# Performance work log

Hardware: AMD Instinct MI355X
Metric: run time of the kernel (lower is better)

The kernel has to match this reference:

```python
import jax, jax.numpy as jnp
import numpy as np

D_MODEL = 1024
N_HEADS = 16
HEAD_DIM = D_MODEL // N_HEADS
WINDOW = 256
NEG_INF = -1e30  # finite stand-in for -inf; identical softmax result, NaN-safe


def setup_inputs() -> dict:
    key = jax.random.key(0)
    ks = jax.random.split(key, 5)
    B, L = 1, 4096
    s = 1.0 / np.sqrt(D_MODEL)
    return {
        "x": jax.random.normal(ks[0], (B, L, D_MODEL), dtype=jnp.float32),
        "Wq": jax.random.normal(ks[1], (D_MODEL, D_MODEL), dtype=jnp.float32) * s,
        "Wk": jax.random.normal(ks[2], (D_MODEL, D_MODEL), dtype=jnp.float32) * s,
        "Wv": jax.random.normal(ks[3], (D_MODEL, D_MODEL), dtype=jnp.float32) * s,
        "Wo": jax.random.normal(ks[4], (D_MODEL, D_MODEL), dtype=jnp.float32) * s,
    }


def reference(x, Wq, Wk, Wv, Wo):
    B, L, _ = x.shape
    # projections (nn.Linear applies x @ W.T; weights here are stored as [out,in])
    q = (x @ Wq.T).reshape(B, L, N_HEADS, HEAD_DIM).transpose(0, 2, 1, 3)  # [B,H,L,Dh]
    k = (x @ Wk.T).reshape(B, L, N_HEADS, HEAD_DIM).transpose(0, 2, 1, 3)
    v = (x @ Wv.T).reshape(B, L, N_HEADS, HEAD_DIM).transpose(0, 2, 1, 3)

    # sliding-window causal mask: position i attends to j in [i-WINDOW+1, i]
    i = jnp.arange(L)[:, None]
    j = jnp.arange(L)[None, :]
    allowed = (j <= i) & (j >= i - WINDOW + 1)  # [L,L] bool

    scale = 1.0 / jnp.sqrt(jnp.asarray(HEAD_DIM, dtype=q.dtype))
    scores = jnp.einsum("bhqd,bhkd->bhqk", q, k) * scale  # [B,H,L,L]
    scores = jnp.where(allowed, scores, NEG_INF)
    attn = jax.nn.softmax(scores, axis=-1)
    out = jnp.einsum("bhqk,bhkd->bhqd", attn, v)  # [B,H,L,Dh]
    out = out.transpose(0, 2, 1, 3).reshape(B, L, D_MODEL)
    return out @ Wo.T
```

## Files before the change

kernel.cpp:

```cpp
#include <hip/hip_runtime.h>

using bf16x8 = __attribute__((ext_vector_type(8))) short;
using u16x8  = __attribute__((ext_vector_type(8))) unsigned short;
using f32x4  = __attribute__((ext_vector_type(4))) float;

#define LSEQ   4096
#define NH     16
#define DH     64
#define WIN    256
#define DM     1024

__device__ __forceinline__ void gl2lds16(const void* g, void* l) {
  __builtin_amdgcn_global_load_lds(
      (const __attribute__((address_space(1))) unsigned int*)g,
      (__attribute__((address_space(3))) unsigned int*)l,
      16, 0, 0);
}

__device__ __forceinline__ unsigned short f2bf(float f) {
  unsigned int u = __float_as_uint(f);
  u += 0x7fffu + ((u >> 16) & 1u);
  return (unsigned short)(u >> 16);
}

__global__ __launch_bounds__(256) void cvt_all(
    const float* __restrict__ x,  const float* __restrict__ wq,
    const float* __restrict__ wk, const float* __restrict__ wv,
    const float* __restrict__ wo, unsigned short* __restrict__ dst)
{
  const size_t i = ((size_t)blockIdx.x * 256 + threadIdx.x) * 8;
  const size_t XN = (size_t)LSEQ * DM;
  const float* src;
  size_t off;
  if (i < XN) { src = x; off = i; }
  else {
    const size_t j = i - XN;
    const int s = (int)(j >> 20);
    off = j & ((1u << 20) - 1);
    src = (s == 0) ? wq : (s == 1) ? wk : (s == 2) ? wv : wo;
  }
  const f32x4 f0 = *(const f32x4*)(src + off);
  const f32x4 f1 = *(const f32x4*)(src + off + 4);
  u16x8 o;
  o[0] = f2bf(f0[0]); o[1] = f2bf(f0[1]); o[2] = f2bf(f0[2]); o[3] = f2bf(f0[3]);
  o[4] = f2bf(f1[0]); o[5] = f2bf(f1[1]); o[6] = f2bf(f1[2]); o[7] = f2bf(f1[3]);
  *(u16x8*)(dst + i) = o;
}

__device__ __forceinline__ void gemm_tile(
    const unsigned short* __restrict__ X,
    const unsigned short* __restrict__ W,
    int m0, int n0,
    unsigned short* As, unsigned short* Bs,
    f32x4 (&acc)[4][4])
{
  const int tid  = threadIdx.x;
  const int lane = tid & 63;
  const int wave = tid >> 6;
  const int wm = wave >> 1, wn = wave & 1;
  const int fr = lane & 15, quad = lane >> 4;

  const f32x4 zero = {0.f, 0.f, 0.f, 0.f};
  #pragma unroll
  for (int i = 0; i < 4; ++i)
    #pragma unroll
    for (int j = 0; j < 4; ++j)
      acc[i][j] = zero;

  const int c0 = tid, c1 = tid + 256;
  const unsigned short* xa0 = X + (size_t)(m0 + (c0 >> 2)) * DM + (c0 & 3) * 8;
  const unsigned short* xa1 = X + (size_t)(m0 + (c1 >> 2)) * DM + (c1 & 3) * 8;
  const unsigned short* wb0 = W + (size_t)(n0 + (c0 >> 2)) * DM + (c0 & 3) * 8;
  const unsigned short* wb1 = W + (size_t)(n0 + (c1 >> 2)) * DM + (c1 & 3) * 8;
  char* la0 = (char*)As + c0 * 16;
  char* la1 = (char*)As + c1 * 16;
  char* lb0 = (char*)Bs + c0 * 16;
  char* lb1 = (char*)Bs + c1 * 16;

  for (int kt = 0; kt < DM; kt += 32) {
    gl2lds16(xa0 + kt, la0);
    gl2lds16(xa1 + kt, la1);
    gl2lds16(wb0 + kt, lb0);
    gl2lds16(wb1 + kt, lb1);
    __syncthreads();

    bf16x8 a[4], b[4];
    #pragma unroll
    for (int t = 0; t < 4; ++t)
      a[t] = *(const bf16x8*)(As + (wm * 64 + t * 16 + fr) * 32 + quad * 8);
    #pragma unroll
    for (int t = 0; t < 4; ++t)
      b[t] = *(const bf16x8*)(Bs + (wn * 64 + t * 16 + fr) * 32 + quad * 8);

    #pragma unroll
    for (int i = 0; i < 4; ++i)
      #pragma unroll
      for (int j = 0; j < 4; ++j)
        acc[i][j] = __builtin_amdgcn_mfma_f32_16x16x32_bf16(a[i], b[j], acc[i][j], 0, 0, 0);
    __syncthreads();
  }
}

__global__ __launch_bounds__(256) void proj_gemm(
    const unsigned short* __restrict__ X,
    const unsigned short* __restrict__ Wq,
    const unsigned short* __restrict__ Wk,
    const unsigned short* __restrict__ Wv,
    unsigned short* __restrict__ Qo,
    unsigned short* __restrict__ Ko,
    unsigned short* __restrict__ Vt)
{
  __shared__ unsigned short As[128 * 32];
  __shared__ unsigned short Bs[128 * 32];
  const int id = blockIdx.x;
  const int lane = threadIdx.x & 63;
  const int wave = threadIdx.x >> 6;
  const int wm = wave >> 1, wn = wave & 1;
  const int cn = lane & 15, quad = lane >> 4;
  f32x4 acc[4][4];

  if (id < 512) {
    const int m0   = (id & 31) * 128;
    const int by   = id >> 5;
    const int wsel = by >> 3;
    const int n0   = (by & 7) * 128;
    gemm_tile(X, wsel ? Wk : Wq, m0, n0, As, Bs, acc);

    const float qscl = wsel ? 1.0f : 0.180336881f;
    unsigned short* O = wsel ? Ko : Qo;
    #pragma unroll
    for (int i = 0; i < 4; ++i)
      #pragma unroll
      for (int j = 0; j < 4; ++j)
        #pragma unroll
        for (int r = 0; r < 4; ++r) {
          const int row = m0 + wm * 64 + i * 16 + quad * 4 + r;
          const int col = n0 + wn * 64 + j * 16 + cn;
          const int h = col >> 6, d = col & 63;
          O[(size_t)(h * LSEQ + row) * DH + d] = f2bf(acc[i][j][r] * qscl);
        }
  } else {
    const int vid = id - 512;
    const int m0 = (vid & 7) * 128;
    const int n0 = (vid >> 3) * 128;
    gemm_tile(Wv, X, m0, n0, As, Bs, acc);

    #pragma unroll
    for (int i = 0; i < 4; ++i)
      #pragma unroll
      for (int j = 0; j < 4; ++j)
        #pragma unroll
        for (int r = 0; r < 4; ++r) {
          const int row = m0 + wm * 64 + i * 16 + quad * 4 + r;
          const int col = n0 + wn * 64 + j * 16 + cn;
          Vt[(size_t)row * LSEQ + col] = f2bf(acc[i][j][r]);
        }
  }
}

__global__ __launch_bounds__(256) void out_gemm(
    const unsigned short* __restrict__ X,
    const unsigned short* __restrict__ W,
    float* __restrict__ O)
{
  __shared__ unsigned short As2[64 * 32];
  __shared__ unsigned short Bs[128 * 32];
  const int m0 = blockIdx.x * 64;
  const int n0 = blockIdx.y * 128;
  const int tid  = threadIdx.x;
  const int lane = tid & 63;
  const int wave = tid >> 6;
  const int wm = wave >> 1, wn = wave & 1;
  const int fr = lane & 15, quad = lane >> 4;

  const f32x4 zero = {0.f, 0.f, 0.f, 0.f};
  f32x4 acc[2][4];
  #pragma unroll
  for (int i = 0; i < 2; ++i)
    #pragma unroll
    for (int j = 0; j < 4; ++j)
      acc[i][j] = zero;

  const unsigned short* xa  = X + (size_t)(m0 + (tid >> 2)) * DM + (tid & 3) * 8;
  const unsigned short* wb0 = W + (size_t)(n0 + (tid >> 2)) * DM + (tid & 3) * 8;
  const unsigned short* wb1 = W + (size_t)(n0 + ((tid + 256) >> 2)) * DM + (tid & 3) * 8;
  char* la  = (char*)As2 + tid * 16;
  char* lb0 = (char*)Bs + tid * 16;
  char* lb1 = (char*)Bs + (tid + 256) * 16;

  for (int kt = 0; kt < DM; kt += 32) {
    gl2lds16(xa + kt, la);
    gl2lds16(wb0 + kt, lb0);
    gl2lds16(wb1 + kt, lb1);
    __syncthreads();

    bf16x8 a[2], b[4];
    #pragma unroll
    for (int t = 0; t < 2; ++t)
      a[t] = *(const bf16x8*)(As2 + (wm * 32 + t * 16 + fr) * 32 + quad * 8);
    #pragma unroll
    for (int t = 0; t < 4; ++t)
      b[t] = *(const bf16x8*)(Bs + (wn * 64 + t * 16 + fr) * 32 + quad * 8);

    #pragma unroll
    for (int i = 0; i < 2; ++i)
      #pragma unroll
      for (int j = 0; j < 4; ++j)
        acc[i][j] = __builtin_amdgcn_mfma_f32_16x16x32_bf16(a[i], b[j], acc[i][j], 0, 0, 0);
    __syncthreads();
  }

  const int cn = lane & 15;
  #pragma unroll
  for (int i = 0; i < 2; ++i)
    #pragma unroll
    for (int j = 0; j < 4; ++j)
      #pragma unroll
      for (int r = 0; r < 4; ++r) {
        const int row = m0 + wm * 32 + i * 16 + quad * 4 + r;
        const int col = n0 + wn * 64 + j * 16 + cn;
        O[(size_t)row * DM + col] = acc[i][j][r];
      }
}

#define PSTR 72
__global__ __launch_bounds__(256) void attn_fwd(
    const unsigned short* __restrict__ Q,
    const unsigned short* __restrict__ K,
    const unsigned short* __restrict__ Vt,
    unsigned short* __restrict__ Oa)
{
  __shared__ unsigned short Ks[2][64 * PSTR];
  __shared__ unsigned short Vs[2][64 * PSTR];
  __shared__ unsigned short Pl[4][16 * PSTR];
  const int id   = blockIdx.x;
  const int h    = (id & 7) | ((id >> 9) << 3);
  const int bq0  = ((id >> 3) & 63) * 64;
  const int tid  = threadIdx.x;
  const int wave = tid >> 6;
  const int lane = tid & 63;
  const int n = lane & 15, quad = lane >> 4;
  const int q0 = bq0 + wave * 16;
  unsigned short* pl = Pl[wave];

  const size_t qbase = ((size_t)(h * LSEQ + q0 + n)) * DH + quad * 8;
  const bf16x8 aq0 = *(const bf16x8*)(Q + qbase);
  const bf16x8 aq1 = *(const bf16x8*)(Q + qbase + 32);

  const int lo = (bq0 >= WIN) ? (bq0 - WIN) : 0;

  const int c0 = tid, c1 = tid + 256;
  const size_t kg0 = ((size_t)(h * LSEQ + (c0 >> 3))) * DH + (c0 & 7) * 8;
  const size_t kg1 = ((size_t)(h * LSEQ + (c1 >> 3))) * DH + (c1 & 7) * 8;
  const size_t vg0 = ((size_t)(h * DH + (c0 >> 3))) * LSEQ + (c0 & 7) * 8;
  const size_t vg1 = ((size_t)(h * DH + (c1 >> 3))) * LSEQ + (c1 & 7) * 8;
  const int ld0 = (c0 >> 3) * PSTR + (c0 & 7) * 8;
  const int ld1 = (c1 >> 3) * PSTR + (c1 & 7) * 8;

  {
    const bf16x8 ka = *(const bf16x8*)(K  + kg0 + (size_t)lo * DH);
    const bf16x8 kc = *(const bf16x8*)(K  + kg1 + (size_t)lo * DH);
    const bf16x8 va = *(const bf16x8*)(Vt + vg0 + lo);
    const bf16x8 vc = *(const bf16x8*)(Vt + vg1 + lo);
    *(bf16x8*)(Ks[0] + ld0) = ka;
    *(bf16x8*)(Ks[0] + ld1) = kc;
    *(bf16x8*)(Vs[0] + ld0) = va;
    *(bf16x8*)(Vs[0] + ld1) = vc;
  }
  __syncthreads();

  const f32x4 zero = {0.f, 0.f, 0.f, 0.f};
  f32x4 acc[4] = {zero, zero, zero, zero};
  float li[4] = {0.f, 0.f, 0.f, 0.f};

  int t = 0;
  for (int jb = lo; jb < bq0 + 64; jb += 64, ++t) {
    const int buf = t & 1;
    const bool more = (jb + 64 < bq0 + 64);
    bf16x8 nk0, nk1, nv0, nv1;
    if (more) {
      const int jn = jb + 64;
      nk0 = *(const bf16x8*)(K  + kg0 + (size_t)jn * DH);
      nk1 = *(const bf16x8*)(K  + kg1 + (size_t)jn * DH);
      nv0 = *(const bf16x8*)(Vt + vg0 + jn);
      nv1 = *(const bf16x8*)(Vt + vg1 + jn);
    }
    const unsigned short* ks = Ks[buf];
    const unsigned short* vs = Vs[buf];
    f32x4 s[4];
    #pragma unroll
    for (int u = 0; u < 4; ++u) {
      const bf16x8 kb0 = *(const bf16x8*)(ks + (u * 16 + n) * PSTR + quad * 8);
      const bf16x8 kb1 = *(const bf16x8*)(ks + (u * 16 + n) * PSTR + 32 + quad * 8);
      f32x4 c = zero;
      c = __builtin_amdgcn_mfma_f32_16x16x32_bf16(aq0, kb0, c, 0, 0, 0);
      c = __builtin_amdgcn_mfma_f32_16x16x32_bf16(aq1, kb1, c, 0, 0, 0);
      s[u] = c;
    }
    #pragma unroll
    for (int u = 0; u < 4; ++u)
      #pragma unroll
      for (int r = 0; r < 4; ++r) {
        const int qi = q0 + quad * 4 + r;
        const int kj = jb + u * 16 + n;
        const bool ok = (kj <= qi) && (kj + WIN > qi);
        const float e = __builtin_exp2f(ok ? s[u][r] - 32.0f : -1e30f);
        s[u][r] = e;
        li[r] += e;
      }
    #pragma unroll
    for (int u = 0; u < 4; ++u)
      #pragma unroll
      for (int r = 0; r < 4; ++r)
        pl[(quad * 4 + r) * PSTR + u * 16 + n] = f2bf(s[u][r]);
    asm volatile("s_waitcnt lgkmcnt(0)" ::: "memory");
    const bf16x8 pa0 = *(const bf16x8*)(pl + n * PSTR + quad * 8);
    const bf16x8 pa1 = *(const bf16x8*)(pl + n * PSTR + 32 + quad * 8);
    #pragma unroll
    for (int ct = 0; ct < 4; ++ct) {
      const bf16x8 vb0 = *(const bf16x8*)(vs + (ct * 16 + n) * PSTR + quad * 8);
      const bf16x8 vb1 = *(const bf16x8*)(vs + (ct * 16 + n) * PSTR + 32 + quad * 8);
      acc[ct] = __builtin_amdgcn_mfma_f32_16x16x32_bf16(pa0, vb0, acc[ct], 0, 0, 0);
      acc[ct] = __builtin_amdgcn_mfma_f32_16x16x32_bf16(pa1, vb1, acc[ct], 0, 0, 0);
    }
    if (more) {
      *(bf16x8*)(Ks[buf ^ 1] + ld0) = nk0;
      *(bf16x8*)(Ks[buf ^ 1] + ld1) = nk1;
      *(bf16x8*)(Vs[buf ^ 1] + ld0) = nv0;
      *(bf16x8*)(Vs[buf ^ 1] + ld1) = nv1;
    }
    __syncthreads();
  }

  float rd[4];
  #pragma unroll
  for (int r = 0; r < 4; ++r) {
    float v = li[r];
    v += __shfl_xor(v, 1);
    v += __shfl_xor(v, 2);
    v += __shfl_xor(v, 4);
    v += __shfl_xor(v, 8);
    rd[r] = 1.0f / v;
  }
  #pragma unroll
  for (int ct = 0; ct < 4; ++ct)
    #pragma unroll
    for (int r = 0; r < 4; ++r) {
      const int row = q0 + quad * 4 + r;
      const int col = h * DH + ct * 16 + n;
      Oa[(size_t)row * DM + col] = f2bf(acc[ct][r] * rd[r]);
    }
}

extern "C" void kernel_launch(void* const* d_in, const int* in_sizes, int n_in,
                              void* d_out, int out_size, void* d_ws, size_t ws_size,
                              hipStream_t stream) {
  const float* x  = (const float*)d_in[0];
  const float* Wq = (const float*)d_in[1];
  const float* Wk = (const float*)d_in[2];
  const float* Wv = (const float*)d_in[3];
  const float* Wo = (const float*)d_in[4];
  float* out = (float*)d_out;

  unsigned short* xb  = (unsigned short*)d_ws;
  unsigned short* Wqb = xb  + (size_t)LSEQ * DM;
  unsigned short* Wkb = Wqb + (size_t)DM * DM;
  unsigned short* Wvb = Wkb + (size_t)DM * DM;
  unsigned short* Wob = Wvb + (size_t)DM * DM;
  unsigned short* Q    = Wob + (size_t)DM * DM;
  unsigned short* K    = Q   + (size_t)LSEQ * DM;
  unsigned short* Vt   = K   + (size_t)LSEQ * DM;
  unsigned short* Attn = Vt  + (size_t)LSEQ * DM;

  cvt_all<<<dim3(4096), 256, 0, stream>>>(x, Wq, Wk, Wv, Wo, xb);
  proj_gemm<<<dim3(768), 256, 0, stream>>>(xb, Wqb, Wkb, Wvb, Q, K, Vt);
  attn_fwd<<<dim3(1024), 256, 0, stream>>>(Q, K, Vt, Attn);
  out_gemm<<<dim3(64, 8), 256, 0, stream>>>(Attn, Wob, out);
}
```

Baseline: 156.5 us.

## Enlarge attention query tile to 128 with per-wave block skipping; reuse 128x128 GEMM tile

The attention kernel now processes 128 queries per block with 8 waves, so each K/V tile loaded into shared memory is shared by twice as many query rows. Waves skip key blocks that fall entirely outside their window and take a mask-free exp path on blocks that need no masking. The output projection switches to the shared 128x128 gemm_tile helper, halving its grid. The trade-off is fewer, larger blocks (512 attention, 256 out-GEMM), which lowers the number of concurrent blocks and leaves some waves idle at barriers while others compute.

```diff
diff --git a/kernel.cpp b/kernel.cpp
--- a/kernel.cpp
+++ b/kernel.cpp
@@ -163,68 +163,32 @@
     const unsigned short* __restrict__ W,
     float* __restrict__ O)
 {
-  __shared__ unsigned short As2[64 * 32];
+  __shared__ unsigned short As[128 * 32];
   __shared__ unsigned short Bs[128 * 32];
-  const int m0 = blockIdx.x * 64;
+  const int m0 = blockIdx.x * 128;
   const int n0 = blockIdx.y * 128;
-  const int tid  = threadIdx.x;
-  const int lane = tid & 63;
-  const int wave = tid >> 6;
+  const int lane = threadIdx.x & 63;
+  const int wave = threadIdx.x >> 6;
   const int wm = wave >> 1, wn = wave & 1;
-  const int fr = lane & 15, quad = lane >> 4;
-
-  const f32x4 zero = {0.f, 0.f, 0.f, 0.f};
-  f32x4 acc[2][4];
+  const int cn = lane & 15, quad = lane >> 4;
+  f32x4 acc[4][4];
+
+  gemm_tile(X, W, m0, n0, As, Bs, acc);
+
   #pragma unroll
-  for (int i = 0; i < 2; ++i)
+  for (int i = 0; i < 4; ++i)
     #pragma unroll
     for (int j = 0; j < 4; ++j)
-      acc[i][j] = zero;
-
-  const unsigned short* xa  = X + (size_t)(m0 + (tid >> 2)) * DM + (tid & 3) * 8;
-  const unsigned short* wb0 = W + (size_t)(n0 + (tid >> 2)) * DM + (tid & 3) * 8;
-  const unsigned short* wb1 = W + (size_t)(n0 + ((tid + 256) >> 2)) * DM + (tid & 3) * 8;
-  char* la  = (char*)As2 + tid * 16;
-  char* lb0 = (char*)Bs + tid * 16;
-  char* lb1 = (char*)Bs + (tid + 256) * 16;
-
-  for (int kt = 0; kt < DM; kt += 32) {
-    gl2lds16(xa + kt, la);
-    gl2lds16(wb0 + kt, lb0);
-    gl2lds16(wb1 + kt, lb1);
-    __syncthreads();
-
-    bf16x8 a[2], b[4];
-    #pragma unroll
-    for (int t = 0; t < 2; ++t)
-      a[t] = *(const bf16x8*)(As2 + (wm * 32 + t * 16 + fr) * 32 + quad * 8);
-    #pragma unroll
-    for (int t = 0; t < 4; ++t)
-      b[t] = *(const bf16x8*)(Bs + (wn * 64 + t * 16 + fr) * 32 + quad * 8);
-
-    #pragma unroll
-    for (int i = 0; i < 2; ++i)
-      #pragma unroll
-      for (int j = 0; j < 4; ++j)
-        acc[i][j] = __builtin_amdgcn_mfma_f32_16x16x32_bf16(a[i], b[j], acc[i][j], 0, 0, 0);
-    __syncthreads();
-  }
-
-  const int cn = lane & 15;
-  #pragma unroll
-  for (int i = 0; i < 2; ++i)
-    #pragma unroll
-    for (int j = 0; j < 4; ++j)
       #pragma unroll
       for (int r = 0; r < 4; ++r) {
-        const int row = m0 + wm * 32 + i * 16 + quad * 4 + r;
+        const int row = m0 + wm * 64 + i * 16 + quad * 4 + r;
         const int col = n0 + wn * 64 + j * 16 + cn;
         O[(size_t)row * DM + col] = acc[i][j][r];
       }
 }
 
 #define PSTR 72
-__global__ __launch_bounds__(256) void attn_fwd(
+__global__ __launch_bounds__(512) void attn_fwd(
     const unsigned short* __restrict__ Q,
     const unsigned short* __restrict__ K,
     const unsigned short* __restrict__ Vt,
@@ -232,10 +196,10 @@
 {
   __shared__ unsigned short Ks[2][64 * PSTR];
   __shared__ unsigned short Vs[2][64 * PSTR];
-  __shared__ unsigned short Pl[4][16 * PSTR];
+  __shared__ unsigned short Pl[8][16 * PSTR];
   const int id   = blockIdx.x;
-  const int h    = (id & 7) | ((id >> 9) << 3);
-  const int bq0  = ((id >> 3) & 63) * 64;
+  const int h    = (id & 7) | ((id >> 8) << 3);
+  const int bq0  = ((id >> 3) & 31) * 128;
   const int tid  = threadIdx.x;
   const int wave = tid >> 6;
   const int lane = tid & 63;
@@ -248,24 +212,16 @@
   const bf16x8 aq1 = *(const bf16x8*)(Q + qbase + 32);
 
   const int lo = (bq0 >= WIN) ? (bq0 - WIN) : 0;
-
-  const int c0 = tid, c1 = tid + 256;
-  const size_t kg0 = ((size_t)(h * LSEQ + (c0 >> 3))) * DH + (c0 & 7) * 8;
-  const size_t kg1 = ((size_t)(h * LSEQ + (c1 >> 3))) * DH + (c1 & 7) * 8;
-  const size_t vg0 = ((size_t)(h * DH + (c0 >> 3))) * LSEQ + (c0 & 7) * 8;
-  const size_t vg1 = ((size_t)(h * DH + (c1 >> 3))) * LSEQ + (c1 & 7) * 8;
-  const int ld0 = (c0 >> 3) * PSTR + (c0 & 7) * 8;
-  const int ld1 = (c1 >> 3) * PSTR + (c1 & 7) * 8;
+  const int hi = bq0 + 128;
+
+  const int krow = tid >> 3, part = tid & 7;
+  const size_t kg = ((size_t)(h * LSEQ + krow)) * DH + part * 8;
+  const size_t vg = ((size_t)(h * DH + krow)) * LSEQ + part * 8;
+  const int ld = krow * PSTR + part * 8;
 
   {
-    const bf16x8 ka = *(const bf16x8*)(K  + kg0 + (size_t)lo * DH);
-    const bf16x8 kc = *(const bf16x8*)(K  + kg1 + (size_t)lo * DH);
-    const bf16x8 va = *(const bf16x8*)(Vt + vg0 + lo);
-    const bf16x8 vc = *(const bf16x8*)(Vt + vg1 + lo);
-    *(bf16x8*)(Ks[0] + ld0) = ka;
-    *(bf16x8*)(Ks[0] + ld1) = kc;
-    *(bf16x8*)(Vs[0] + ld0) = va;
-    *(bf16x8*)(Vs[0] + ld1) = vc;
+    *(bf16x8*)(Ks[0] + ld) = *(const bf16x8*)(K  + kg + (size_t)lo * DH);
+    *(bf16x8*)(Vs[0] + ld) = *(const bf16x8*)(Vt + vg + lo);
   }
   __syncthreads();
 
@@ -274,60 +230,70 @@
   float li[4] = {0.f, 0.f, 0.f, 0.f};
 
   int t = 0;
-  for (int jb = lo; jb < bq0 + 64; jb += 64, ++t) {
+  for (int jb = lo; jb < hi; jb += 64, ++t) {
     const int buf = t & 1;
-    const bool more = (jb + 64 < bq0 + 64);
-    bf16x8 nk0, nk1, nv0, nv1;
+    const bool more = (jb + 64 < hi);
+    bf16x8 nk, nv;
     if (more) {
-      const int jn = jb + 64;
-      nk0 = *(const bf16x8*)(K  + kg0 + (size_t)jn * DH);
-      nk1 = *(const bf16x8*)(K  + kg1 + (size_t)jn * DH);
-      nv0 = *(const bf16x8*)(Vt + vg0 + jn);
-      nv1 = *(const bf16x8*)(Vt + vg1 + jn);
+      nk = *(const bf16x8*)(K  + kg + (size_t)(jb + 64) * DH);
+      nv = *(const bf16x8*)(Vt + vg + (jb + 64));
     }
-    const unsigned short* ks = Ks[buf];
-    const unsigned short* vs = Vs[buf];
-    f32x4 s[4];
-    #pragma unroll
-    for (int u = 0; u < 4; ++u) {
-      const bf16x8 kb0 = *(const bf16x8*)(ks + (u * 16 + n) * PSTR + quad * 8);
-      const bf16x8 kb1 = *(const bf16x8*)(ks + (u * 16 + n) * PSTR + 32 + quad * 8);
-      f32x4 c = zero;
-      c = __builtin_amdgcn_mfma_f32_16x16x32_bf16(aq0, kb0, c, 0, 0, 0);
-      c = __builtin_amdgcn_mfma_f32_16x16x32_bf16(aq1, kb1, c, 0, 0, 0);
-      s[u] = c;
-    }
-    #pragma unroll
-    for (int u = 0; u < 4; ++u)
-      #pragma unroll
-      for (int r = 0; r < 4; ++r) {
-        const int qi = q0 + quad * 4 + r;
-        const int kj = jb + u * 16 + n;
-        const bool ok = (kj <= qi) && (kj + WIN > qi);
-        const float e = __builtin_exp2f(ok ? s[u][r] - 32.0f : -1e30f);
-        s[u][r] = e;
-        li[r] += e;
+    const bool active = (jb <= q0 + 15) && (jb + 63 >= q0 - (WIN - 1));
+    if (active) {
+      const unsigned short* ks = Ks[buf];
+      const unsigned short* vs = Vs[buf];
+      f32x4 s[4];
+      #pragma unroll
+      for (int u = 0; u < 4; ++u) {
+        const bf16x8 kb0 = *(const bf16x8*)(ks + (u * 16 + n) * PSTR + quad * 8);
+        const bf16x8 kb1 = *(const bf16x8*)(ks + (u * 16 + n) * PSTR + 32 + quad * 8);
+        f32x4 c = zero;
+        c = __builtin_amdgcn_mfma_f32_16x16x32_bf16(aq0, kb0, c, 0, 0, 0);
+        c = __builtin_amdgcn_mfma_f32_16x16x32_bf16(aq1, kb1, c, 0, 0, 0);
+        s[u] = c;
       }
-    #pragma unroll
-    for (int u = 0; u < 4; ++u)
-      #pragma unroll
-      for (int r = 0; r < 4; ++r)
-        pl[(quad * 4 + r) * PSTR + u * 16 + n] = f2bf(s[u][r]);
-    asm volatile("s_waitcnt lgkmcnt(0)" ::: "memory");
-    const bf16x8 pa0 = *(const bf16x8*)(pl + n * PSTR + quad * 8);
-    const bf16x8 pa1 = *(const bf16x8*)(pl + n * PSTR + 32 + quad * 8);
-    #pragma unroll
-    for (int ct = 0; ct < 4; ++ct) {
-      const bf16x8 vb0 = *(const bf16x8*)(vs + (ct * 16 + n) * PSTR + quad * 8);
-      const bf16x8 vb1 = *(const bf16x8*)(vs + (ct * 16 + n) * PSTR + 32 + quad * 8);
-      acc[ct] = __builtin_amdgcn_mfma_f32_16x16x32_bf16(pa0, vb0, acc[ct], 0, 0, 0);
-      acc[ct] = __builtin_amdgcn_mfma_f32_16x16x32_bf16(pa1, vb1, acc[ct], 0, 0, 0);
+      const bool nomask = (jb + 63 <= q0) && (jb >= q0 + 15 - (WIN - 1));
+      if (nomask) {
+        #pragma unroll
+        for (int u = 0; u < 4; ++u)
+          #pragma unroll
+          for (int r = 0; r < 4; ++r) {
+            const float e = __builtin_exp2f(s[u][r] - 32.0f);
+            s[u][r] = e;
+            li[r] += e;
+          }
+      } else {
+        #pragma unroll
+        for (int u = 0; u < 4; ++u)
+          #pragma unroll
+          for (int r = 0; r < 4; ++r) {
+            const int qi = q0 + quad * 4 + r;
+            const int kj = jb + u * 16 + n;
+            const bool ok = (kj <= qi) && (kj + WIN > qi);
+            const float e = __builtin_exp2f(ok ? s[u][r] - 32.0f : -1e30f);
+            s[u][r] = e;
+            li[r] += e;
+          }
+      }
+      #pragma unroll
+      for (int u = 0; u < 4; ++u)
+        #pragma unroll
+        for (int r = 0; r < 4; ++r)
+          pl[(quad * 4 + r) * PSTR + u * 16 + n] = f2bf(s[u][r]);
+      asm volatile("s_waitcnt lgkmcnt(0)" ::: "memory");
+      const bf16x8 pa0 = *(const bf16x8*)(pl + n * PSTR + quad * 8);
+      const bf16x8 pa1 = *(const bf16x8*)(pl + n * PSTR + 32 + quad * 8);
+      #pragma unroll
+      for (int ct = 0; ct < 4; ++ct) {
+        const bf16x8 vb0 = *(const bf16x8*)(vs + (ct * 16 + n) * PSTR + quad * 8);
+        const bf16x8 vb1 = *(const bf16x8*)(vs + (ct * 16 + n) * PSTR + 32 + quad * 8);
+        acc[ct] = __builtin_amdgcn_mfma_f32_16x16x32_bf16(pa0, vb0, acc[ct], 0, 0, 0);
+        acc[ct] = __builtin_amdgcn_mfma_f32_16x16x32_bf16(pa1, vb1, acc[ct], 0, 0, 0);
+      }
     }
     if (more) {
-      *(bf16x8*)(Ks[buf ^ 1] + ld0) = nk0;
-      *(bf16x8*)(Ks[buf ^ 1] + ld1) = nk1;
-      *(bf16x8*)(Vs[buf ^ 1] + ld0) = nv0;
-      *(bf16x8*)(Vs[buf ^ 1] + ld1) = nv1;
+      *(bf16x8*)(Ks[buf ^ 1] + ld) = nk;
+      *(bf16x8*)(Vs[buf ^ 1] + ld) = nv;
     }
     __syncthreads();
   }
@@ -374,6 +340,6 @@
 
   cvt_all<<<dim3(4096), 256, 0, stream>>>(x, Wq, Wk, Wv, Wo, xb);
   proj_gemm<<<dim3(768), 256, 0, stream>>>(xb, Wqb, Wkb, Wvb, Q, K, Vt);
-  attn_fwd<<<dim3(1024), 256, 0, stream>>>(Q, K, Vt, Attn);
-  out_gemm<<<dim3(64, 8), 256, 0, stream>>>(Attn, Wob, out);
-}
+  attn_fwd<<<dim3(512), 512, 0, stream>>>(Q, K, Vt, Attn);
+  out_gemm<<<dim3(32, 8), 256, 0, stream>>>(Attn, Wob, out);
+}
```

New measurement: 160.1 us. 1.02x slower.
